# Optimization experiments

Measured on AMD Instinct MI355X. Metric: run time of the kernel, lower is better.

## Reference

```python
import jax, jax.numpy as jnp
import numpy as np

B, P, EPG = 1000, 100, 1200  # graphs, nodes/graph, edges/graph
IN, HID, OUT, K = 16, 64, 5, 3


def setup_inputs() -> dict:
    key = jax.random.key(0)
    ks = jax.random.split(key, 12)
    offs = jnp.repeat(jnp.arange(B, dtype=jnp.int32) * P, EPG)
    src = jax.random.randint(ks[0], (B * EPG,), 0, P, dtype=jnp.int32) + offs
    dst = jax.random.randint(ks[1], (B * EPG,), 0, P, dtype=jnp.int32) + offs
    graph_ids = jnp.repeat(jnp.arange(B, dtype=jnp.int32), P)
    feat = jax.random.normal(ks[2], (B * P, IN), dtype=jnp.float32)

    def lin(k1, fan_in, fan_out):
        s = 1.0 / np.sqrt(fan_in)
        return jax.random.uniform(k1, (fan_in, fan_out), jnp.float32, -s, s)

    return {
        'feat': feat, 'src': src, 'dst': dst, 'graph_ids': graph_ids,
        'n_graphs': B,
        'W1': lin(ks[3], K * IN, HID), 'b1': jnp.zeros((HID,), jnp.float32),
        'W2': lin(ks[4], K * HID, HID), 'b2': jnp.zeros((HID,), jnp.float32),
        'W3': lin(ks[5], K * HID, HID), 'b3': jnp.zeros((HID,), jnp.float32),
        'Wfc': lin(ks[6], HID, OUT), 'bfc': jnp.zeros((OUT,), jnp.float32),
    }


def _cheb_conv(x, src, dst, d_invsqrt, W, b, k):
    # DGL ChebConv with lambda_max=2 -> re_norm=1, scaled Laplacian = -D^-1/2 A D^-1/2
    n = x.shape[0]

    def Ax(h):
        msg = (h * d_invsqrt)[src]                      # gather from source nodes
        agg = jax.ops.segment_sum(msg, dst, num_segments=n)
        return agg * d_invsqrt

    Xs = [x]
    if k > 1:
        Xs.append(-Ax(Xs[0]))                           # X1 = L_hat X0
        for _ in range(2, k):
            Xs.append(-2.0 * Ax(Xs[-1]) - Xs[-2])       # X_i = 2 L_hat X_{i-1} - X_{i-2}
    Xt = jnp.concatenate(Xs, axis=1)                    # [n, k*f]
    return Xt @ W + b


def reference(feat, src, dst, graph_ids, n_graphs, W1, b1, W2, b2, W3, b3, Wfc, bfc):
    n = feat.shape[0]
    deg = jax.ops.segment_sum(jnp.ones((src.shape[0],), feat.dtype), dst, num_segments=n)
    d_invsqrt = jnp.where(deg < 1.0, 1.0, deg) ** -0.5
    d_invsqrt = d_invsqrt[:, None]

    h = jax.nn.relu(_cheb_conv(feat, src, dst, d_invsqrt, W1, b1, K))
    h = jax.nn.relu(_cheb_conv(h, src, dst, d_invsqrt, W2, b2, K))
    h = jax.nn.relu(_cheb_conv(h, src, dst, d_invsqrt, W3, b3, K))

    # dgl.mean_nodes: per-graph mean pooling
    counts = jax.ops.segment_sum(jnp.ones((n,), h.dtype), graph_ids, num_segments=n_graphs)
    hg = jax.ops.segment_sum(h, graph_ids, num_segments=n_graphs) / counts[:, None]
    return hg @ Wfc + bfc
```

## Files before the change

kernel.cpp:

```cpp
#include <hip/hip_runtime.h>

#define NGRAPH 1000
#define P      100
#define EPG    1200
#define INF    16
#define HID    64
#define NOUT   5


#define ASTR   100
#define DINVC  64
#define DEGC   65
#define T1OFF  68
#define T2OFF  84

#define AINT_K   128
#define AINT_SZ  (P * AINT_K)

#define RK1    64
#define RK2    208
#define L1HI   0
#define L1LO   4096
#define L2HI   8192
#define L2LO   21504
#define L3HI   34816
#define L3LO   48128
#define WT_SHORTS 61440

typedef short short8 __attribute__((ext_vector_type(8)));
typedef float f32x4  __attribute__((ext_vector_type(4)));

__device__ __forceinline__ void bsplit(float x, short& h, short& l) {
    unsigned u = __float_as_uint(x);
    h = (short)(u >> 16);
    float hf = __uint_as_float(u & 0xffff0000u);
    l = (short)(__float_as_uint(x - hf) >> 16);
}

__global__ __launch_bounds__(256) void prep(
    const float* __restrict__ W1, const float* __restrict__ W2,
    const float* __restrict__ W3, short* __restrict__ wt,
    const int* __restrict__ src, const int* __restrict__ dst,
    short* __restrict__ aint)
{
    const int tid = threadIdx.x;
    {
        const int i0 = blockIdx.x * blockDim.x + tid;
        const int stride = gridDim.x * blockDim.x;
        for (int e = i0; e < HID * RK1; e += stride) {
            int c = e / RK1, r = e % RK1;
            float v = (r < 3 * INF) ? W1[r * HID + c] : 0.f;
            short h, l; bsplit(v, h, l);
            wt[L1HI + e] = h;
            wt[L1LO + e] = l;
        }
        for (int e = i0; e < HID * RK2; e += stride) {
            int c = e / RK2, r = e % RK2;
            float v2 = (r < 3 * HID) ? W2[r * HID + c] : 0.f;
            float v3 = (r < 3 * HID) ? W3[r * HID + c] : 0.f;
            short h, l;
            bsplit(v2, h, l); wt[L2HI + e] = h; wt[L2LO + e] = l;
            bsplit(v3, h, l); wt[L3HI + e] = h; wt[L3LO + e] = l;
        }
    }
    __shared__ unsigned int cnt[AINT_SZ / 2];
    const int g = blockIdx.x, base = g * P;
    for (int i = tid; i < AINT_SZ / 2; i += 256) cnt[i] = 0u;
    __syncthreads();
    const int* srcg = src + g * EPG;
    const int* dstg = dst + g * EPG;
    for (int e = tid; e < EPG; e += 256) {
        int s = srcg[e] - base;
        int d = dstg[e] - base;
        int idx = d * AINT_K + s;
        atomicAdd(&cnt[idx >> 1], 1u << ((idx & 1) * 16));
    }
    __syncthreads();
    unsigned int* outw = (unsigned int*)(aint + (size_t)g * AINT_SZ);
    for (int i = tid; i < AINT_SZ / 2; i += 256) {
        unsigned int u = cnt[i];
        unsigned int b0 = __float_as_uint((float)(u & 0xffffu)) >> 16;
        unsigned int b1 = __float_as_uint((float)(u >> 16)) >> 16;
        outw[i] = b0 | (b1 << 16);
    }
}

template <int SECOND>
__device__ __forceinline__ void dense_prop(
    float* __restrict__ A, const short* __restrict__ aintg,
    int arow0, int arow1, bool has2,
    int srcoff, int dstoff, int ycol,
    int rb0, int rb1, f32x4 dv0, f32x4 dv1, int lane)
{
    const int n16 = lane & 15;
    const int q   = lane >> 4;
    const int kq  = q * 8;
    f32x4 p0, p1;
    p0[0]=0.f; p0[1]=0.f; p0[2]=0.f; p0[3]=0.f;
    p1[0]=0.f; p1[1]=0.f; p1[2]=0.f; p1[3]=0.f;
#pragma unroll
    for (int k = 0; k < 4; k++) {
        const short8 a0 = *(const short8*)&aintg[arow0 * AINT_K + k * 32 + kq];
        const short8 a1 = *(const short8*)&aintg[arow1 * AINT_K + k * 32 + kq];
        short8 bhi, blo; short h, l;
#pragma unroll
        for (int j = 0; j < 8; j++) {
            int row = k * 32 + kq + j;
            if (k == 3) row = (row < P) ? row : 0;
            float x = A[row * ASTR + srcoff + n16];
            bsplit(x, h, l); bhi[j] = h; blo[j] = l;
        }
        p0 = __builtin_amdgcn_mfma_f32_16x16x32_bf16(a0, bhi, p0, 0, 0, 0);
        p0 = __builtin_amdgcn_mfma_f32_16x16x32_bf16(a0, blo, p0, 0, 0, 0);
        if (has2) {
            p1 = __builtin_amdgcn_mfma_f32_16x16x32_bf16(a1, bhi, p1, 0, 0, 0);
            p1 = __builtin_amdgcn_mfma_f32_16x16x32_bf16(a1, blo, p1, 0, 0, 0);
        }
    }
#pragma unroll
    for (int r = 0; r < 4; r++) {
        const int row = rb0 + q * 4 + r;
        const float d2 = dv0[r] * dv0[r];
        float o;
        if (SECOND) o = -2.f * d2 * p0[r] - A[row * ASTR + ycol];
        else        o = -d2 * p0[r];
        A[row * ASTR + dstoff + n16] = o;
    }
    if (has2) {
#pragma unroll
        for (int r = 0; r < 4; r++) {
            const int row = rb1 + q * 4 + r;
            if (rb1 != 84 || row >= 96) {
                const float d2 = dv1[r] * dv1[r];
                float o;
                if (SECOND) o = -2.f * d2 * p1[r] - A[row * ASTR + ycol];
                else        o = -d2 * p1[r];
                A[row * ASTR + dstoff + n16] = o;
            }
        }
    }
}

template <int F, int FINAL>
__device__ __forceinline__ void cheb_layer(
    float* __restrict__ A, const short* __restrict__ aintg,
    const short* __restrict__ whi, const short* __restrict__ wlo,
    const float* __restrict__ bias,
    int tid, int rb0, int rb1, bool has2, f32x4 dv0, f32x4 dv1)
{
    const int RK   = 3 * F + 16;
    const int lane = tid & 63;
    const int wv   = tid >> 6;
    const int n16  = lane & 15;
    const int q    = lane >> 4;
    const int ncol = (wv << 4) + n16;

    const int arow0 = rb0 + n16;
    const int arow1 = (has2 ? rb1 : rb0) + n16;

    f32x4 acc[7];
#pragma unroll
    for (int t = 0; t < 7; t++) { acc[t][0]=0.f; acc[t][1]=0.f; acc[t][2]=0.f; acc[t][3]=0.f; }

    for (int cb = 0; cb < F; cb += 16) {
        dense_prop<0>(A, aintg, arow0, arow1, has2, cb,    T1OFF, 0,
                      rb0, rb1, dv0, dv1, lane);
        __syncthreads();
        dense_prop<1>(A, aintg, arow0, arow1, has2, T1OFF, T2OFF, cb + n16,
                      rb0, rb1, dv0, dv1, lane);
        __syncthreads();

#pragma unroll
        for (int ks = 0; ks < 2; ks++) {
            int wr, aoff;
            if (ks == 0) {
                wr   = (q == 0) ? cb : (q == 1) ? cb + 8 : (q == 2) ? F + cb : F + cb + 8;
                aoff = (q == 0) ? cb : (q == 1) ? cb + 8 : (q == 2) ? T1OFF  : T1OFF + 8;
            } else {
                wr   = (q == 0) ? 2*F + cb : (q == 1) ? 2*F + cb + 8 : (q == 2) ? 3*F : 3*F + 8;
                aoff = (q == 0) ? T2OFF    : (q == 1) ? T2OFF + 8    : (q == 2) ? T1OFF : T1OFF + 8;
            }
            const short8 bhi = *(const short8*)&whi[ncol * RK + wr];
            const short8 blo = *(const short8*)&wlo[ncol * RK + wr];
#pragma unroll
            for (int t = 0; t < 7; t++) {
                const int row = ((t < 6) ? t * 16 : 84) + n16;
                const float* xp = &A[row * ASTR + aoff];
                const float4 v0 = *(const float4*)xp;
                const float4 v1 = *(const float4*)(xp + 4);
                short8 ahi, alo; short h, l;
                bsplit(v0.x, h, l); ahi[0] = h; alo[0] = l;
                bsplit(v0.y, h, l); ahi[1] = h; alo[1] = l;
                bsplit(v0.z, h, l); ahi[2] = h; alo[2] = l;
                bsplit(v0.w, h, l); ahi[3] = h; alo[3] = l;
                bsplit(v1.x, h, l); ahi[4] = h; alo[4] = l;
                bsplit(v1.y, h, l); ahi[5] = h; alo[5] = l;
                bsplit(v1.z, h, l); ahi[6] = h; alo[6] = l;
                bsplit(v1.w, h, l); ahi[7] = h; alo[7] = l;
                acc[t] = __builtin_amdgcn_mfma_f32_16x16x32_bf16(ahi, bhi, acc[t], 0, 0, 0);
                acc[t] = __builtin_amdgcn_mfma_f32_16x16x32_bf16(ahi, blo, acc[t], 0, 0, 0);
                acc[t] = __builtin_amdgcn_mfma_f32_16x16x32_bf16(alo, bhi, acc[t], 0, 0, 0);
            }
        }
        __syncthreads();
    }

    const float bcol = bias[ncol];
#pragma unroll
    for (int t = 0; t < 7; t++) {
        const int rbase = ((t < 6) ? t * 16 : 84) + q * 4;
#pragma unroll
        for (int r = 0; r < 4; r++) {
            const int row = rbase + r;
            if (t < 6 || row >= 96) {
                const float dn = A[row * ASTR + DINVC];
                const float v = acc[t][r];
                float o;
                if (FINAL) o = fmaxf(v * (1.0f / dn) + bcol, 0.f);
                else       o = fmaxf(v + bcol * dn, 0.f);
                A[row * ASTR + ncol] = o;
            }
        }
    }
    __syncthreads();
}

__global__ __launch_bounds__(256, 4) void gnn_kernel(
    const float* __restrict__ feat,
    const int* __restrict__ src, const int* __restrict__ dst,
    const float* __restrict__ b1, const float* __restrict__ b2,
    const float* __restrict__ b3,
    const float* __restrict__ Wfc, const float* __restrict__ bfc,
    const short* __restrict__ wt, const short* __restrict__ aint,
    float* __restrict__ out)
{
    __shared__ __align__(16) float A[P * ASTR];
    const int g = blockIdx.x;
    const int tid = threadIdx.x;
    const int base = g * P;
    const int* dstg = dst + g * EPG;

    for (int i = tid; i < P; i += 256) *(int*)&A[i * ASTR + DEGC] = 0;
    __syncthreads();
    for (int e = tid; e < EPG; e += 256) {
        int d = dstg[e] - base;
        atomicAdd((int*)&A[d * ASTR + DEGC], 1);
    }
    __syncthreads();
    for (int i = tid; i < P; i += 256) {
        int dg = *(int*)&A[i * ASTR + DEGC];
        A[i * ASTR + DINVC] = rsqrtf((float)(dg > 1 ? dg : 1));
    }
    __syncthreads();

    for (int i = tid; i < P * INF / 4; i += 256) {
        int n = i >> 2, fq = (i & 3) * 4;
        float4 v = *(const float4*)&feat[(size_t)base * INF + i * 4];
        float dn = A[n * ASTR + DINVC];
        v.x *= dn; v.y *= dn; v.z *= dn; v.w *= dn;
        *(float4*)&A[n * ASTR + fq] = v;
    }
    __syncthreads();

    const int lane = tid & 63, wv = tid >> 6, q = lane >> 4;
    const int rb0 = wv * 16;
    const int t2i = wv + 4;
    const int rb1 = (t2i >= 6) ? 84 : t2i * 16;
    const bool has2 = (wv < 3);
    f32x4 dv0, dv1;
#pragma unroll
    for (int r = 0; r < 4; r++) {
        dv0[r] = A[(rb0 + q * 4 + r) * ASTR + DINVC];
        dv1[r] = A[((has2 ? rb1 : rb0) + q * 4 + r) * ASTR + DINVC];
    }

    const short* aintg = aint + (size_t)g * AINT_SZ;
    cheb_layer<INF, 0>(A, aintg, wt + L1HI, wt + L1LO, b1, tid, rb0, rb1, has2, dv0, dv1);
    cheb_layer<HID, 0>(A, aintg, wt + L2HI, wt + L2LO, b2, tid, rb0, rb1, has2, dv0, dv1);
    cheb_layer<HID, 1>(A, aintg, wt + L3HI, wt + L3LO, b3, tid, rb0, rb1, has2, dv0, dv1);

    {
        const int l2 = tid & 63, w = tid >> 6;
        float s = 0.f;
        for (int n = w; n < P; n += 4) s += A[n * ASTR + l2];
        A[l2 * ASTR + T1OFF + w] = s;
    }
    __syncthreads();
    if (tid < HID) {
        float hg = (A[tid * ASTR + T1OFF] + A[tid * ASTR + T1OFF + 1] +
                    A[tid * ASTR + T1OFF + 2] + A[tid * ASTR + T1OFF + 3]) * (1.0f / P);
        A[tid * ASTR + T1OFF + 4] = hg;
    }
    __syncthreads();
    if (tid < NOUT) {
        float o = bfc[tid];
        for (int c = 0; c < HID; c++) o += A[c * ASTR + T1OFF + 4] * Wfc[c * NOUT + tid];
        out[g * NOUT + tid] = o;
    }
}

extern "C" void kernel_launch(void* const* d_in, const int* in_sizes, int n_in,
                              void* d_out, int out_size, void* d_ws, size_t ws_size,
                              hipStream_t stream)
{
    const float* feat = (const float*)d_in[0];
    const int*   src  = (const int*)d_in[1];
    const int*   dst  = (const int*)d_in[2];
    const float* W1  = (const float*)d_in[5];
    const float* b1  = (const float*)d_in[6];
    const float* W2  = (const float*)d_in[7];
    const float* b2  = (const float*)d_in[8];
    const float* W3  = (const float*)d_in[9];
    const float* b3  = (const float*)d_in[10];
    const float* Wfc = (const float*)d_in[11];
    const float* bfc = (const float*)d_in[12];
    float* out = (float*)d_out;

    short* wt   = (short*)d_ws;
    short* aint = wt + WT_SHORTS;

    prep<<<NGRAPH, 256, 0, stream>>>(W1, W2, W3, wt, src, dst, aint);
    gnn_kernel<<<NGRAPH, 256, 0, stream>>>(feat, src, dst,
                                           b1, b2, b3, Wfc, bfc, wt, aint, out);
}
```

Baseline: 159.4 us.

## Partition MFMA output tiles by rows across waves instead of by columns

The dense Chebyshev GEMM was split so each of the four waves owned a 16-column slice and converted all seven 16-row A tiles to hi/lo bf16. Now waves 0-2 each own two row tiles and wave 3 owns the last tile, and every wave computes all four column tiles. Each A tile is therefore loaded from LDS and split only once across the block, rather than once per wave. The cost is more weight loads from global/L2, since each wave now reads all columns. Work is also unbalanced: wave 3 does half the MFMAs of the other waves.

```diff
diff --git a/kernel.cpp b/kernel.cpp
--- a/kernel.cpp
+++ b/kernel.cpp
@@ -153,14 +153,18 @@
     const int wv   = tid >> 6;
     const int n16  = lane & 15;
     const int q    = lane >> 4;
-    const int ncol = (wv << 4) + n16;
 
     const int arow0 = rb0 + n16;
     const int arow1 = (has2 ? rb1 : rb0) + n16;
 
-    f32x4 acc[7];
-#pragma unroll
-    for (int t = 0; t < 7; t++) { acc[t][0]=0.f; acc[t][1]=0.f; acc[t][2]=0.f; acc[t][3]=0.f; }
+    const bool two  = (wv < 3);
+    const int t0    = two ? wv * 2 : 6;
+    const int rbo0  = (t0 < 6) ? t0 * 16 : 84;
+    const int rbo1  = rbo0 + 16;
+
+    f32x4 acc[8];
+#pragma unroll
+    for (int i = 0; i < 8; i++) { acc[i][0]=0.f; acc[i][1]=0.f; acc[i][2]=0.f; acc[i][3]=0.f; }
 
     for (int cb = 0; cb < F; cb += 16) {
         dense_prop<0>(A, aintg, arow0, arow1, has2, cb,    T1OFF, 0,
@@ -180,41 +184,74 @@
                 wr   = (q == 0) ? 2*F + cb : (q == 1) ? 2*F + cb + 8 : (q == 2) ? 3*F : 3*F + 8;
                 aoff = (q == 0) ? T2OFF    : (q == 1) ? T2OFF + 8    : (q == 2) ? T1OFF : T1OFF + 8;
             }
-            const short8 bhi = *(const short8*)&whi[ncol * RK + wr];
-            const short8 blo = *(const short8*)&wlo[ncol * RK + wr];
-#pragma unroll
-            for (int t = 0; t < 7; t++) {
-                const int row = ((t < 6) ? t * 16 : 84) + n16;
-                const float* xp = &A[row * ASTR + aoff];
+            short8 ahi0, alo0; short h, l;
+            {
+                const float* xp = &A[(rbo0 + n16) * ASTR + aoff];
                 const float4 v0 = *(const float4*)xp;
                 const float4 v1 = *(const float4*)(xp + 4);
-                short8 ahi, alo; short h, l;
-                bsplit(v0.x, h, l); ahi[0] = h; alo[0] = l;
-                bsplit(v0.y, h, l); ahi[1] = h; alo[1] = l;
-                bsplit(v0.z, h, l); ahi[2] = h; alo[2] = l;
-                bsplit(v0.w, h, l); ahi[3] = h; alo[3] = l;
-                bsplit(v1.x, h, l); ahi[4] = h; alo[4] = l;
-                bsplit(v1.y, h, l); ahi[5] = h; alo[5] = l;
-                bsplit(v1.z, h, l); ahi[6] = h; alo[6] = l;
-                bsplit(v1.w, h, l); ahi[7] = h; alo[7] = l;
-                acc[t] = __builtin_amdgcn_mfma_f32_16x16x32_bf16(ahi, bhi, acc[t], 0, 0, 0);
-                acc[t] = __builtin_amdgcn_mfma_f32_16x16x32_bf16(ahi, blo, acc[t], 0, 0, 0);
-                acc[t] = __builtin_amdgcn_mfma_f32_16x16x32_bf16(alo, bhi, acc[t], 0, 0, 0);
+                bsplit(v0.x, h, l); ahi0[0] = h; alo0[0] = l;
+                bsplit(v0.y, h, l); ahi0[1] = h; alo0[1] = l;
+                bsplit(v0.z, h, l); ahi0[2] = h; alo0[2] = l;
+                bsplit(v0.w, h, l); ahi0[3] = h; alo0[3] = l;
+                bsplit(v1.x, h, l); ahi0[4] = h; alo0[4] = l;
+                bsplit(v1.y, h, l); ahi0[5] = h; alo0[5] = l;
+                bsplit(v1.z, h, l); ahi0[6] = h; alo0[6] = l;
+                bsplit(v1.w, h, l); ahi0[7] = h; alo0[7] = l;
+            }
+            short8 ahi1, alo1;
+            if (two) {
+                const float* xp = &A[(rbo1 + n16) * ASTR + aoff];
+                const float4 v0 = *(const float4*)xp;
+                const float4 v1 = *(const float4*)(xp + 4);
+                bsplit(v0.x, h, l); ahi1[0] = h; alo1[0] = l;
+                bsplit(v0.y, h, l); ahi1[1] = h; alo1[1] = l;
+                bsplit(v0.z, h, l); ahi1[2] = h; alo1[2] = l;
+                bsplit(v0.w, h, l); ahi1[3] = h; alo1[3] = l;
+                bsplit(v1.x, h, l); ahi1[4] = h; alo1[4] = l;
+                bsplit(v1.y, h, l); ahi1[5] = h; alo1[5] = l;
+                bsplit(v1.z, h, l); ahi1[6] = h; alo1[6] = l;
+                bsplit(v1.w, h, l); ahi1[7] = h; alo1[7] = l;
+            }
+#pragma unroll
+            for (int nt = 0; nt < 4; nt++) {
+                const int ncol = nt * 16 + n16;
+                const short8 bhi = *(const short8*)&whi[ncol * RK + wr];
+                const short8 blo = *(const short8*)&wlo[ncol * RK + wr];
+                acc[nt] = __builtin_amdgcn_mfma_f32_16x16x32_bf16(ahi0, bhi, acc[nt], 0, 0, 0);
+                acc[nt] = __builtin_amdgcn_mfma_f32_16x16x32_bf16(ahi0, blo, acc[nt], 0, 0, 0);
+                acc[nt] = __builtin_amdgcn_mfma_f32_16x16x32_bf16(alo0, bhi, acc[nt], 0, 0, 0);
+                if (two) {
+                    acc[4+nt] = __builtin_amdgcn_mfma_f32_16x16x32_bf16(ahi1, bhi, acc[4+nt], 0, 0, 0);
+                    acc[4+nt] = __builtin_amdgcn_mfma_f32_16x16x32_bf16(ahi1, blo, acc[4+nt], 0, 0, 0);
+                    acc[4+nt] = __builtin_amdgcn_mfma_f32_16x16x32_bf16(alo1, bhi, acc[4+nt], 0, 0, 0);
+                }
             }
         }
         __syncthreads();
     }
 
-    const float bcol = bias[ncol];
-#pragma unroll
-    for (int t = 0; t < 7; t++) {
-        const int rbase = ((t < 6) ? t * 16 : 84) + q * 4;
+#pragma unroll
+    for (int nt = 0; nt < 4; nt++) {
+        const int ncol = nt * 16 + n16;
+        const float bcol = bias[ncol];
 #pragma unroll
         for (int r = 0; r < 4; r++) {
-            const int row = rbase + r;
-            if (t < 6 || row >= 96) {
+            const int row = rbo0 + q * 4 + r;
+            if (t0 < 6 || row >= 96) {
                 const float dn = A[row * ASTR + DINVC];
-                const float v = acc[t][r];
+                const float v = acc[nt][r];
+                float o;
+                if (FINAL) o = fmaxf(v * (1.0f / dn) + bcol, 0.f);
+                else       o = fmaxf(v + bcol * dn, 0.f);
+                A[row * ASTR + ncol] = o;
+            }
+        }
+        if (two) {
+#pragma unroll
+            for (int r = 0; r < 4; r++) {
+                const int row = rbo1 + q * 4 + r;
+                const float dn = A[row * ASTR + DINVC];
+                const float v = acc[4+nt][r];
                 float o;
                 if (FINAL) o = fmaxf(v * (1.0f / dn) + bcol, 0.f);
                 else       o = fmaxf(v + bcol * dn, 0.f);
```

New measurement: 171.5 us. 7.6% more time.
